# Kernel optimization log

Hardware: AMD Instinct MI355X
Metric: run time of the kernel (lower is better)

## Reference

```python
import jax, jax.numpy as jnp
import numpy as np

B, S, D = 4, 2048, 1024
H = 16
HD = D // H  # 64
BASE = 10000.0


def _rope_cache(seq_len, dim):
    inv_freq = 1.0 / (BASE ** (jnp.arange(0, dim, 2, dtype=jnp.float32) / dim))
    t = jnp.arange(seq_len, dtype=jnp.float32)
    freqs = jnp.einsum('i,j->ij', t, inv_freq)          # [S, dim/2]
    emb = jnp.concatenate([freqs, freqs], axis=-1)      # [S, dim]
    return jnp.cos(emb), jnp.sin(emb)


def _rotate_half(x):
    x1, x2 = jnp.split(x, 2, axis=-1)
    return jnp.concatenate([-x2, x1], axis=-1)


def setup_inputs() -> dict:
    key = jax.random.key(0)
    ks = jax.random.split(key, 5)
    scale = 1.0 / np.sqrt(D)
    return {
        'x': jax.random.normal(ks[0], (B, S, D), dtype=jnp.float32),
        'Wq': jax.random.normal(ks[1], (D, D), dtype=jnp.float32) * scale,
        'Wk': jax.random.normal(ks[2], (D, D), dtype=jnp.float32) * scale,
        'Wv': jax.random.normal(ks[3], (D, D), dtype=jnp.float32) * scale,
        'Wo': jax.random.normal(ks[4], (D, D), dtype=jnp.float32) * scale,
    }


def reference(x, Wq, Wk, Wv, Wo):
    b, s, d = x.shape
    # projections (torch Linear, no bias): y = x @ W.T
    q = (x @ Wq.T).reshape(b, s, H, HD).transpose(0, 2, 1, 3)  # [B,H,S,HD]
    k = (x @ Wk.T).reshape(b, s, H, HD).transpose(0, 2, 1, 3)
    v = (x @ Wv.T).reshape(b, s, H, HD).transpose(0, 2, 1, 3)
    cos, sin = _rope_cache(s, HD)  # [S, HD]
    cos = cos[None, None]
    sin = sin[None, None]
    q = q * cos + _rotate_half(q) * sin
    k = k * cos + _rotate_half(k) * sin
    scale = 1.0 / np.sqrt(HD)
    attn = jnp.einsum('bhqd,bhkd->bhqk', q, k) * scale  # [B,H,S,S]
    attn = jax.nn.softmax(attn, axis=-1)
    out = jnp.einsum('bhqk,bhkd->bhqd', attn, v)
    out = out.transpose(0, 2, 1, 3).reshape(b, s, d)
    return out @ Wo.T
```

## Files before the change

### kernel.cpp

```cpp
#include <hip/hip_runtime.h>
#include <math.h>
#include <stdint.h>

#define BB 4
#define SS 2048
#define DDIM 1024
#define HH 16
#define HD 64
#define QKVLD 3072
#define QSCALE (0.125f * 1.44269504089f)

typedef __bf16 bf16x8 __attribute__((ext_vector_type(8)));
typedef float f32x4 __attribute__((ext_vector_type(4)));
typedef float f32x16 __attribute__((ext_vector_type(16)));
typedef int i32x4 __attribute__((ext_vector_type(4)));

__device__ __forceinline__ unsigned short f2bf(float f) {
    union { float f; unsigned u; } v; v.f = f;
    unsigned r = (v.u + 0x7FFFu + ((v.u >> 16) & 1u)) >> 16;
    return (unsigned short)r;
}
__device__ __forceinline__ void gload_lds16(const unsigned short* g, unsigned char* s) {
    __builtin_amdgcn_global_load_lds(
        (const __attribute__((address_space(1))) unsigned int*)(g),
        (__attribute__((address_space(3))) unsigned int*)(s), 16, 0, 0);
}

__global__ void prep_all(const float* __restrict__ x,
                         const float* __restrict__ Wq, const float* __restrict__ Wk,
                         const float* __restrict__ Wv, const float* __restrict__ Wo,
                         unsigned short* __restrict__ xb,
                         unsigned short* __restrict__ wqkv, unsigned short* __restrict__ wob,
                         float* __restrict__ cosT, float* __restrict__ sinT) {
    int bid = blockIdx.x;
    if (bid < 8192) {
        int i = bid * 256 + threadIdx.x;
        float4 v = ((const float4*)x)[i];
        ushort4 o;
        o.x = f2bf(v.x); o.y = f2bf(v.y); o.z = f2bf(v.z); o.w = f2bf(v.w);
        ((ushort4*)xb)[i] = o;
    } else if (bid < 12288) {
        int i = (bid - 8192) * 256 + threadIdx.x;
        int mat = i >> 18;
        int off = i & 262143;
        const float* src = (mat == 0) ? Wq : (mat == 1) ? Wk : (mat == 2) ? Wv : Wo;
        unsigned short* dst = (mat < 3) ? (wqkv + (size_t)mat * 1048576) : wob;
        float4 v = ((const float4*)src)[off];
        ushort4 o;
        o.x = f2bf(v.x); o.y = f2bf(v.y); o.z = f2bf(v.z); o.w = f2bf(v.w);
        ((ushort4*)dst)[off] = o;
    } else {
        int idx = (bid - 12288) * 256 + threadIdx.x;
        int s = idx >> 5;
        int j = idx & 31;
        float invf = powf(10000.0f, -(float)j / 32.0f);
        float ang = (float)s * invf;
        cosT[idx] = cosf(ang);
        sinT[idx] = sinf(ang);
    }
}

__global__ __launch_bounds__(512) void gemm256_qkv(const unsigned short* __restrict__ A,
                                                   const unsigned short* __restrict__ Bm,
                                                   unsigned short* __restrict__ C,
                                                   const float* __restrict__ cosT,
                                                   const float* __restrict__ sinT,
                                                   unsigned short* __restrict__ vt) {
    __shared__ unsigned char smem[131072];
    const int t = threadIdx.x;
    const int l = t & 63;
    const int w = t >> 6;
    const int wm = w >> 2;
    const int wn = w & 3;
    const int K = DDIM;
    const int NT = K >> 6;

    const int bid = blockIdx.y * gridDim.x + blockIdx.x;
    const int cpx = (gridDim.x * gridDim.y) >> 3;
    const int swz = (bid & 7) * cpx + (bid >> 3);
    const int row0 = (swz / gridDim.x) * 256;
    const int col0 = (swz % gridDim.x) * 256;

    f32x4 acc[8][4];
#pragma unroll
    for (int i = 0; i < 8; ++i)
#pragma unroll
        for (int j = 0; j < 4; ++j) acc[i][j] = f32x4{0.f, 0.f, 0.f, 0.f};

    const unsigned short* aSg = A + (size_t)(row0 + w * 16 + (l >> 3)) * K + ((l & 7) ^ (l >> 3)) * 8;
    const unsigned short* bSg = Bm + (size_t)(col0 + w * 16 + (l >> 3)) * K + ((l & 7) ^ (l >> 3)) * 8;
    const int dRow = (w * 16) * 128;

#define STAGE_A(kt, h, j, buf) \
    gload_lds16(aSg + (size_t)((h) * 128 + (j) * 8) * K + (kt) * 64, \
                smem + (buf) * 65536 + (h) * 16384 + dRow + (j) * 1024)
#define STAGE_B(kt, h, j, buf) \
    gload_lds16(bSg + (size_t)((h) * 128 + (j) * 8) * K + (kt) * 64, \
                smem + (buf) * 65536 + 32768 + (h) * 16384 + dRow + (j) * 1024)

    STAGE_B(0, 0, 0, 0); STAGE_B(0, 0, 1, 0); STAGE_B(0, 1, 0, 0); STAGE_B(0, 1, 1, 0);
    STAGE_A(0, 0, 0, 0); STAGE_A(0, 0, 1, 0); STAGE_A(0, 1, 0, 0); STAGE_A(0, 1, 1, 0);
    STAGE_B(1, 0, 0, 1); STAGE_B(1, 0, 1, 1); STAGE_B(1, 1, 0, 1); STAGE_B(1, 1, 1, 1);
    asm volatile("s_waitcnt vmcnt(4)" ::: "memory");
    __builtin_amdgcn_s_barrier();

    const int cA = (l >> 4) << 4;
    const int swr = (l & 7) << 4;
    const int rA0 = wm * 128 + (l & 15);
    const int rB0 = wn * 64 + (l & 15);

    int cur = 0;
    for (int u = 0; u < NT; ++u) {
        const int nxt = cur ^ 1;
        const unsigned char* Ab = smem + cur * 65536;
        const unsigned char* Bb = smem + cur * 65536 + 32768;
        const bool pA = (u + 1 < NT);
        const bool pB = (u + 2 < NT);
        bf16x8 bfr[4][2];

#pragma unroll
        for (int p = 0; p < 4; ++p) {
            if (p == 0) { if (pA) { STAGE_A(u + 1, 0, 0, nxt); STAGE_A(u + 1, 0, 1, nxt); } }
            if (p == 1) { if (pA) { STAGE_A(u + 1, 1, 0, nxt); STAGE_A(u + 1, 1, 1, nxt); } }
            if (p == 2) { if (pB) { STAGE_B(u + 2, 0, 0, cur); STAGE_B(u + 2, 0, 1, cur); } }
            if (p == 3) { if (pB) { STAGE_B(u + 2, 1, 0, cur); STAGE_B(u + 2, 1, 1, cur); } }

            if (p == 0) {
#pragma unroll
                for (int ni = 0; ni < 4; ++ni)
#pragma unroll
                    for (int kk = 0; kk < 2; ++kk) {
                        int row = rB0 + ni * 16;
                        bfr[ni][kk] = *(const bf16x8*)(Bb + (row * 128 + ((kk * 64 + cA) ^ swr)));
                    }
            }
            bf16x8 af[2][2];
#pragma unroll
            for (int m2 = 0; m2 < 2; ++m2)
#pragma unroll
                for (int kk = 0; kk < 2; ++kk) {
                    int row = rA0 + (p * 2 + m2) * 16;
                    af[m2][kk] = *(const bf16x8*)(Ab + (row * 128 + ((kk * 64 + cA) ^ swr)));
                }

            __builtin_amdgcn_s_barrier();
            asm volatile("s_waitcnt lgkmcnt(0)" ::: "memory");
            __builtin_amdgcn_sched_barrier(0);
            __builtin_amdgcn_s_setprio(1);
#pragma unroll
            for (int m2 = 0; m2 < 2; ++m2)
#pragma unroll
                for (int ni = 0; ni < 4; ++ni)
#pragma unroll
                    for (int kk = 0; kk < 2; ++kk)
                        acc[p * 2 + m2][ni] = __builtin_amdgcn_mfma_f32_16x16x32_bf16(
                            af[m2][kk], bfr[ni][kk], acc[p * 2 + m2][ni], 0, 0, 0);
            __builtin_amdgcn_s_setprio(0);
            if (p == 3) {
                if (u < NT - 2) asm volatile("s_waitcnt vmcnt(4)" ::: "memory");
                else            asm volatile("s_waitcnt vmcnt(0)" ::: "memory");
            }
            __builtin_amdgcn_s_barrier();
        }
        cur = nxt;
    }
#undef STAGE_A
#undef STAGE_B

    const int cr = (l >> 4) << 2;
    const int cc = l & 15;
    const int sec = (col0 + wn * 64) >> 10;

    if (sec == 2) {
#pragma unroll
        for (int mi = 0; mi < 8; ++mi) {
            int s0 = row0 + wm * 128 + mi * 16 + cr;
            int bI = s0 >> 11;
            int sI = s0 & (SS - 1);
#pragma unroll
            for (int ni = 0; ni < 4; ++ni) {
                int vcol = col0 + wn * 64 + ni * 16 + cc - 2048;
                int hh = vcol >> 6, dd = vcol & 63;
                ushort4 o;
                o.x = f2bf(acc[mi][ni][0]);
                o.y = f2bf(acc[mi][ni][1]);
                o.z = f2bf(acc[mi][ni][2]);
                o.w = f2bf(acc[mi][ni][3]);
                *(ushort4*)&vt[((size_t)((bI * HH + hh) * HD + dd)) * SS + sI] = o;
            }
        }
    } else {
        const float qs = (sec == 0) ? QSCALE : 1.0f;
#pragma unroll
        for (int mi = 0; mi < 8; ++mi) {
#pragma unroll
            for (int r = 0; r < 4; ++r) {
                int grow = row0 + wm * 128 + mi * 16 + cr + r;
                int s = grow & (SS - 1);
#pragma unroll
                for (int ni = 0; ni < 2; ++ni) {
                    int j = ni * 16 + cc;
                    float c = cosT[(s << 5) + j];
                    float sn = sinT[(s << 5) + j];
                    float x1 = acc[mi][ni][r], x2 = acc[mi][ni + 2][r];
                    int gcol = col0 + wn * 64 + j;
                    C[(size_t)grow * QKVLD + gcol]      = f2bf((x1 * c - x2 * sn) * qs);
                    C[(size_t)grow * QKVLD + gcol + 32] = f2bf((x2 * c + x1 * sn) * qs);
                }
            }
        }
    }
}

__global__ __launch_bounds__(512) void gemm_out256(const unsigned short* __restrict__ A,
                                                   const unsigned short* __restrict__ Bm,
                                                   float* __restrict__ C) {
    __shared__ unsigned char smem[98304];
    const int t = threadIdx.x;
    const int l = t & 63;
    const int w = t >> 6;
    const int wm = w >> 2;
    const int wn = w & 3;
    const int K = DDIM;
    const int NT = K >> 6;

    const int bid = blockIdx.y * gridDim.x + blockIdx.x;
    const int cpx = (gridDim.x * gridDim.y) >> 3;
    const int swz = (bid & 7) * cpx + (bid >> 3);
    const int row0 = (swz / gridDim.x) * 256;
    const int col0 = (swz % gridDim.x) * 128;

    f32x4 acc[8][2];
#pragma unroll
    for (int i = 0; i < 8; ++i)
#pragma unroll
        for (int j = 0; j < 2; ++j) acc[i][j] = f32x4{0.f, 0.f, 0.f, 0.f};

    const unsigned short* aSg = A + (size_t)(row0 + w * 8 + (l >> 3)) * QKVLD + ((l & 7) ^ (l >> 3)) * 8;
    const unsigned short* bSg = Bm + (size_t)(col0 + w * 8 + (l >> 3)) * K + ((l & 7) ^ (l >> 3)) * 8;
    const int dRow = (w * 8) * 128;

#define SA(kt, c, buf) \
    gload_lds16(aSg + (size_t)((c) * 64) * QKVLD + (kt) * 64, \
                smem + (buf) * 49152 + (c) * 8192 + dRow)
#define SB(kt, c, buf) \
    gload_lds16(bSg + (size_t)((c) * 64) * K + (kt) * 64, \
                smem + (buf) * 49152 + 32768 + (c) * 8192 + dRow)

    SB(0, 0, 0); SB(0, 1, 0);
    SA(0, 0, 0); SA(0, 1, 0); SA(0, 2, 0); SA(0, 3, 0);
    SB(1, 0, 1); SB(1, 1, 1);
    asm volatile("s_waitcnt vmcnt(2)" ::: "memory");
    __builtin_amdgcn_s_barrier();

    const int cA = (l >> 4) << 4;
    const int swr = (l & 7) << 4;
    const int rA0 = wm * 128 + (l & 15);
    const int rB0 = wn * 32 + (l & 15);

    int cur = 0;
    for (int u = 0; u < NT; ++u) {
        const int nxt = cur ^ 1;
        const unsigned char* Ab = smem + cur * 49152;
        const unsigned char* Bb = smem + cur * 49152 + 32768;
        const bool pA = (u + 1 < NT);
        const bool pB = (u + 2 < NT);
        bf16x8 bfr[2][2];

#pragma unroll
        for (int p = 0; p < 4; ++p) {
            if (p == 0) { if (pA) { SA(u + 1, 0, nxt); SA(u + 1, 1, nxt); } }
            if (p == 1) { if (pA) { SA(u + 1, 2, nxt); SA(u + 1, 3, nxt); } }
            if (p == 2) { if (pB) { SB(u + 2, 0, cur); } }
            if (p == 3) { if (pB) { SB(u + 2, 1, cur); } }

            if (p == 0) {
#pragma unroll
                for (int ni = 0; ni < 2; ++ni)
#pragma unroll
                    for (int kk = 0; kk < 2; ++kk) {
                        int row = rB0 + ni * 16;
                        bfr[ni][kk] = *(const bf16x8*)(Bb + (row * 128 + ((kk * 64 + cA) ^ swr)));
                    }
            }
            bf16x8 af[2][2];
#pragma unroll
            for (int m2 = 0; m2 < 2; ++m2)
#pragma unroll
                for (int kk = 0; kk < 2; ++kk) {
                    int row = rA0 + (p * 2 + m2) * 16;
                    af[m2][kk] = *(const bf16x8*)(Ab + (row * 128 + ((kk * 64 + cA) ^ swr)));
                }

            __builtin_amdgcn_s_barrier();
            asm volatile("s_waitcnt lgkmcnt(0)" ::: "memory");
            __builtin_amdgcn_sched_barrier(0);
            __builtin_amdgcn_s_setprio(1);
#pragma unroll
            for (int m2 = 0; m2 < 2; ++m2)
#pragma unroll
                for (int ni = 0; ni < 2; ++ni)
#pragma unroll
                    for (int kk = 0; kk < 2; ++kk)
                        acc[p * 2 + m2][ni] = __builtin_amdgcn_mfma_f32_16x16x32_bf16(
                            af[m2][kk], bfr[ni][kk], acc[p * 2 + m2][ni], 0, 0, 0);
            __builtin_amdgcn_s_setprio(0);
            if (p == 3) {
                if (u < NT - 2) asm volatile("s_waitcnt vmcnt(2)" ::: "memory");
                else            asm volatile("s_waitcnt vmcnt(0)" ::: "memory");
            }
            __builtin_amdgcn_s_barrier();
        }
        cur = nxt;
    }
#undef SA
#undef SB

    const int cr = (l >> 4) << 2;
    const int cc = l & 15;
#pragma unroll
    for (int mi = 0; mi < 8; ++mi)
#pragma unroll
        for (int ni = 0; ni < 2; ++ni) {
            int gcol = col0 + wn * 32 + ni * 16 + cc;
#pragma unroll
            for (int r = 0; r < 4; ++r) {
                int grow = row0 + wm * 128 + mi * 16 + cr + r;
                C[(size_t)grow * DDIM + gcol] = acc[mi][ni][r];
            }
        }
}

__global__ __launch_bounds__(512) void attn_mfma12(const unsigned short* __restrict__ qkv,
                                                   const unsigned short* __restrict__ vt,
                                                   unsigned short* __restrict__ og) {
    __shared__ unsigned char smem[32768];
    const int tid = threadIdx.x;
    const int ln = tid & 63;
    const int w = tid >> 6;
    const int lq = ln & 31;
    const int hi = ln >> 5;

    const int did = blockIdx.x;
    const int b = did & 3;
    const int h = (did >> 2) & 15;
    const int qb0 = (did >> 6) << 8;

    const int headoff = h * HD;
    const size_t bS = (size_t)b * SS;

    bf16x8 qf[4];
    {
        const unsigned short* qsrc = qkv + (bS + qb0 + w * 32 + lq) * QKVLD + headoff + hi * 8;
#pragma unroll
        for (int dc = 0; dc < 4; ++dc)
            qf[dc] = *(const bf16x8*)(qsrc + dc * 16);
    }

    f32x16 oacc[2];
#pragma unroll
    for (int i = 0; i < 2; ++i)
#pragma unroll
        for (int r = 0; r < 16; ++r) oacc[i][r] = 0.f;
    float lsum = 0.f;

    f32x16 fzero;
#pragma unroll
    for (int r = 0; r < 16; ++r) fzero[r] = 0.f;

    const int srow = w * 8 + (ln >> 3);
    const int scol = ((ln & 7) ^ (ln >> 3)) << 3;
    const unsigned short* kbase_g = qkv + bS * QKVLD + 1024 + headoff;
    const unsigned short* vtbase_g = vt + (size_t)(b * HH + h) * HD * SS;

    {
        gload_lds16(kbase_g + (size_t)srow * QKVLD + scol, smem + w * 1024);
        gload_lds16(vtbase_g + (size_t)srow * SS + scol,   smem + 16384 + w * 1024);
    }
    __syncthreads();

#pragma unroll 2
    for (int tkv = 0; tkv < SS / 64; ++tkv) {
        const int cur = tkv & 1;
        const int kcur = cur * 8192;
        const int vcur = 16384 + cur * 8192;
        const int nxt = cur ^ 1;
        const bool pre = (tkv + 1 < SS / 64);
        if (pre) {
            const int kv1 = (tkv + 1) * 64;
            gload_lds16(kbase_g + (size_t)(kv1 + srow) * QKVLD + scol,
                        smem + nxt * 8192 + w * 1024);
            gload_lds16(vtbase_g + (size_t)srow * SS + kv1 + scol,
                        smem + 16384 + nxt * 8192 + w * 1024);
        }

        f32x16 st[2];
#pragma unroll
        for (int kb = 0; kb < 2; ++kb) {
            bf16x8 kf[4];
#pragma unroll
            for (int dc = 0; dc < 4; ++dc) {
                int row = kb * 32 + lq;
                int o = kcur + ((row * 128 + dc * 32 + hi * 16) ^ ((row & 7) << 4));
                kf[dc] = *(const bf16x8*)(smem + o);
            }
            __builtin_amdgcn_s_setprio(1);
            st[kb] = __builtin_amdgcn_mfma_f32_32x32x16_bf16(kf[0], qf[0], fzero, 0, 0, 0);
#pragma unroll
            for (int dc = 1; dc < 4; ++dc)
                st[kb] = __builtin_amdgcn_mfma_f32_32x32x16_bf16(kf[dc], qf[dc], st[kb], 0, 0, 0);
            __builtin_amdgcn_s_setprio(0);
        }

        float pg[32];
#pragma unroll
        for (int j = 0; j < 16; ++j) pg[j] = __builtin_amdgcn_exp2f(st[0][j]);
#pragma unroll
        for (int j = 0; j < 16; ++j) pg[16 + j] = __builtin_amdgcn_exp2f(st[1][j]);

        i32x4 pwv[4];
#pragma unroll
        for (int g = 0; g < 4; ++g) {
            unsigned u0, u1, u2, u3;
            asm("v_cvt_pk_bf16_f32 %0, %1, %2" : "=v"(u0) : "v"(pg[g * 8 + 0]), "v"(pg[g * 8 + 1]));
            asm("v_cvt_pk_bf16_f32 %0, %1, %2" : "=v"(u1) : "v"(pg[g * 8 + 2]), "v"(pg[g * 8 + 3]));
            asm("v_cvt_pk_bf16_f32 %0, %1, %2" : "=v"(u2) : "v"(pg[g * 8 + 4]), "v"(pg[g * 8 + 5]));
            asm("v_cvt_pk_bf16_f32 %0, %1, %2" : "=v"(u3) : "v"(pg[g * 8 + 6]), "v"(pg[g * 8 + 7]));
            asm("v_permlane32_swap_b32 %0, %1" : "+v"(u0), "+v"(u2));
            asm("v_permlane32_swap_b32 %0, %1" : "+v"(u1), "+v"(u3));
            pwv[g][0] = (int)u0; pwv[g][1] = (int)u1; pwv[g][2] = (int)u2; pwv[g][3] = (int)u3;
        }

        float rs;
        {
            float s0 = (pg[0] + pg[1]) + (pg[2] + pg[3]);
            float s1 = (pg[4] + pg[5]) + (pg[6] + pg[7]);
            float s2 = (pg[8] + pg[9]) + (pg[10] + pg[11]);
            float s3 = (pg[12] + pg[13]) + (pg[14] + pg[15]);
            float s4 = (pg[16] + pg[17]) + (pg[18] + pg[19]);
            float s5 = (pg[20] + pg[21]) + (pg[22] + pg[23]);
            float s6 = (pg[24] + pg[25]) + (pg[26] + pg[27]);
            float s7 = (pg[28] + pg[29]) + (pg[30] + pg[31]);
            rs = ((s0 + s1) + (s2 + s3)) + ((s4 + s5) + (s6 + s7));
        }
        rs += __shfl_xor(rs, 32);
        lsum += rs;

        __builtin_amdgcn_s_setprio(1);
#pragma unroll
        for (int dblk = 0; dblk < 2; ++dblk) {
#pragma unroll
            for (int ks = 0; ks < 4; ++ks) {
                int row = dblk * 32 + lq;
                int o = vcur + ((row * 128 + ks * 32 + hi * 16) ^ ((row & 7) << 4));
                bf16x8 vf = *(const bf16x8*)(smem + o);
                oacc[dblk] = __builtin_amdgcn_mfma_f32_32x32x16_bf16(
                    __builtin_bit_cast(bf16x8, pwv[ks]), vf, oacc[dblk], 0, 0, 0);
            }
        }
        __builtin_amdgcn_s_setprio(0);

        __syncthreads();
    }

    {
        float inv = 1.0f / lsum;
#pragma unroll
        for (int r = 0; r < 16; ++r) {
            int crow = (r & 3) + 8 * (r >> 2) + 4 * hi;
            float invr = __shfl(inv, crow);
            int grow = qb0 + w * 32 + crow;
            size_t base = (bS + grow) * QKVLD + headoff + lq;
            og[base]      = f2bf(oacc[0][r] * invr);
            og[base + 32] = f2bf(oacc[1][r] * invr);
        }
    }
}

extern "C" void kernel_launch(void* const* d_in, const int* in_sizes, int n_in,
                              void* d_out, int out_size, void* d_ws, size_t ws_size,
                              hipStream_t stream) {
    const float* x  = (const float*)d_in[0];
    const float* Wq = (const float*)d_in[1];
    const float* Wk = (const float*)d_in[2];
    const float* Wv = (const float*)d_in[3];
    const float* Wo = (const float*)d_in[4];
    float* out = (float*)d_out;

    const size_t BSD = (size_t)BB * SS * DDIM;
    const size_t WSZ = (size_t)DDIM * DDIM;

    unsigned short* xb   = (unsigned short*)d_ws;
    unsigned short* wqkv = xb + BSD;
    unsigned short* wob  = wqkv + 3 * WSZ;
    unsigned short* qkv  = wob + WSZ;
    unsigned short* vt   = qkv + (size_t)BB * SS * QKVLD;
    float* cosT = (float*)(vt + BSD);
    float* sinT = cosT + (size_t)SS * 32;

    hipLaunchKernelGGL(prep_all, dim3(12544), dim3(256), 0, stream,
                       x, Wq, Wk, Wv, Wo, xb, wqkv, wob, cosT, sinT);

    hipLaunchKernelGGL(gemm256_qkv, dim3(QKVLD / 256, BB * SS / 256), dim3(512), 0, stream,
                       xb, wqkv, qkv, cosT, sinT, vt);

    hipLaunchKernelGGL(attn_mfma12, dim3(512), dim3(512), 0, stream, qkv, vt, qkv);

    hipLaunchKernelGGL(gemm_out256, dim3(DDIM / 128, BB * SS / 256), dim3(512), 0, stream,
                       qkv, wob, out);
}
```

Baseline: 180.4 us.

## Shrink QKV GEMM tile to 256x128 with LDS exchange for RoPE pairs

Changes the QKV projection GEMM tile from 256x256 to 256x128, which doubles the grid to 768 blocks, halves the accumulator registers and cuts LDS from 128KB to 96KB. The aim is better occupancy and CU load balance on a 256-CU device, where 384 blocks would leave some CUs idle in the second wave. Because each wave now owns only 32 columns, the two RoPE halves of a head sit in neighbouring waves. The epilogue therefore swaps accumulators through LDS in two synchronized passes, which adds shared-memory traffic and barriers. The smaller tile also lowers arithmetic intensity per global load.

```diff
diff --git a/kernel.cpp b/kernel.cpp
--- a/kernel.cpp
+++ b/kernel.cpp
@@ -60,13 +60,13 @@
     }
 }
 
-__global__ __launch_bounds__(512) void gemm256_qkv(const unsigned short* __restrict__ A,
-                                                   const unsigned short* __restrict__ Bm,
-                                                   unsigned short* __restrict__ C,
-                                                   const float* __restrict__ cosT,
-                                                   const float* __restrict__ sinT,
-                                                   unsigned short* __restrict__ vt) {
-    __shared__ unsigned char smem[131072];
+__global__ __launch_bounds__(512) void gemm128b_qkv(const unsigned short* __restrict__ A,
+                                                    const unsigned short* __restrict__ Bm,
+                                                    unsigned short* __restrict__ C,
+                                                    const float* __restrict__ cosT,
+                                                    const float* __restrict__ sinT,
+                                                    unsigned short* __restrict__ vt) {
+    __shared__ unsigned char smem[98304];
     const int t = threadIdx.x;
     const int l = t & 63;
     const int w = t >> 6;
@@ -79,55 +79,55 @@
     const int cpx = (gridDim.x * gridDim.y) >> 3;
     const int swz = (bid & 7) * cpx + (bid >> 3);
     const int row0 = (swz / gridDim.x) * 256;
-    const int col0 = (swz % gridDim.x) * 256;
-
-    f32x4 acc[8][4];
+    const int col0 = (swz % gridDim.x) * 128;
+
+    f32x4 acc[8][2];
 #pragma unroll
     for (int i = 0; i < 8; ++i)
 #pragma unroll
-        for (int j = 0; j < 4; ++j) acc[i][j] = f32x4{0.f, 0.f, 0.f, 0.f};
-
-    const unsigned short* aSg = A + (size_t)(row0 + w * 16 + (l >> 3)) * K + ((l & 7) ^ (l >> 3)) * 8;
-    const unsigned short* bSg = Bm + (size_t)(col0 + w * 16 + (l >> 3)) * K + ((l & 7) ^ (l >> 3)) * 8;
-    const int dRow = (w * 16) * 128;
-
-#define STAGE_A(kt, h, j, buf) \
-    gload_lds16(aSg + (size_t)((h) * 128 + (j) * 8) * K + (kt) * 64, \
-                smem + (buf) * 65536 + (h) * 16384 + dRow + (j) * 1024)
-#define STAGE_B(kt, h, j, buf) \
-    gload_lds16(bSg + (size_t)((h) * 128 + (j) * 8) * K + (kt) * 64, \
-                smem + (buf) * 65536 + 32768 + (h) * 16384 + dRow + (j) * 1024)
-
-    STAGE_B(0, 0, 0, 0); STAGE_B(0, 0, 1, 0); STAGE_B(0, 1, 0, 0); STAGE_B(0, 1, 1, 0);
-    STAGE_A(0, 0, 0, 0); STAGE_A(0, 0, 1, 0); STAGE_A(0, 1, 0, 0); STAGE_A(0, 1, 1, 0);
-    STAGE_B(1, 0, 0, 1); STAGE_B(1, 0, 1, 1); STAGE_B(1, 1, 0, 1); STAGE_B(1, 1, 1, 1);
-    asm volatile("s_waitcnt vmcnt(4)" ::: "memory");
+        for (int j = 0; j < 2; ++j) acc[i][j] = f32x4{0.f, 0.f, 0.f, 0.f};
+
+    const unsigned short* aSg = A + (size_t)(row0 + w * 8 + (l >> 3)) * K + ((l & 7) ^ (l >> 3)) * 8;
+    const unsigned short* bSg = Bm + (size_t)(col0 + w * 8 + (l >> 3)) * K + ((l & 7) ^ (l >> 3)) * 8;
+    const int dRow = (w * 8) * 128;
+
+#define SA(kt, c, buf) \
+    gload_lds16(aSg + (size_t)((c) * 64) * K + (kt) * 64, \
+                smem + (buf) * 49152 + (c) * 8192 + dRow)
+#define SB(kt, c, buf) \
+    gload_lds16(bSg + (size_t)((c) * 64) * K + (kt) * 64, \
+                smem + (buf) * 49152 + 32768 + (c) * 8192 + dRow)
+
+    SB(0, 0, 0); SB(0, 1, 0);
+    SA(0, 0, 0); SA(0, 1, 0); SA(0, 2, 0); SA(0, 3, 0);
+    SB(1, 0, 1); SB(1, 1, 1);
+    asm volatile("s_waitcnt vmcnt(2)" ::: "memory");
     __builtin_amdgcn_s_barrier();
 
     const int cA = (l >> 4) << 4;
     const int swr = (l & 7) << 4;
     const int rA0 = wm * 128 + (l & 15);
-    const int rB0 = wn * 64 + (l & 15);
+    const int rB0 = wn * 32 + (l & 15);
 
     int cur = 0;
     for (int u = 0; u < NT; ++u) {
         const int nxt = cur ^ 1;
-        const unsigned char* Ab = smem + cur * 65536;
-        const unsigned char* Bb = smem + cur * 65536 + 32768;
+        const unsigned char* Ab = smem + cur * 49152;
+        const unsigned char* Bb = smem + cur * 49152 + 32768;
         const bool pA = (u + 1 < NT);
         const bool pB = (u + 2 < NT);
-        bf16x8 bfr[4][2];
+        bf16x8 bfr[2][2];
 
 #pragma unroll
         for (int p = 0; p < 4; ++p) {
-            if (p == 0) { if (pA) { STAGE_A(u + 1, 0, 0, nxt); STAGE_A(u + 1, 0, 1, nxt); } }
-            if (p == 1) { if (pA) { STAGE_A(u + 1, 1, 0, nxt); STAGE_A(u + 1, 1, 1, nxt); } }
-            if (p == 2) { if (pB) { STAGE_B(u + 2, 0, 0, cur); STAGE_B(u + 2, 0, 1, cur); } }
-            if (p == 3) { if (pB) { STAGE_B(u + 2, 1, 0, cur); STAGE_B(u + 2, 1, 1, cur); } }
+            if (p == 0) { if (pA) { SA(u + 1, 0, nxt); SA(u + 1, 1, nxt); } }
+            if (p == 1) { if (pA) { SA(u + 1, 2, nxt); SA(u + 1, 3, nxt); } }
+            if (p == 2) { if (pB) { SB(u + 2, 0, cur); } }
+            if (p == 3) { if (pB) { SB(u + 2, 1, cur); } }
 
             if (p == 0) {
 #pragma unroll
-                for (int ni = 0; ni < 4; ++ni)
+                for (int ni = 0; ni < 2; ++ni)
 #pragma unroll
                     for (int kk = 0; kk < 2; ++kk) {
                         int row = rB0 + ni * 16;
@@ -150,26 +150,26 @@
 #pragma unroll
             for (int m2 = 0; m2 < 2; ++m2)
 #pragma unroll
-                for (int ni = 0; ni < 4; ++ni)
+                for (int ni = 0; ni < 2; ++ni)
 #pragma unroll
                     for (int kk = 0; kk < 2; ++kk)
                         acc[p * 2 + m2][ni] = __builtin_amdgcn_mfma_f32_16x16x32_bf16(
                             af[m2][kk], bfr[ni][kk], acc[p * 2 + m2][ni], 0, 0, 0);
             __builtin_amdgcn_s_setprio(0);
             if (p == 3) {
-                if (u < NT - 2) asm volatile("s_waitcnt vmcnt(4)" ::: "memory");
+                if (u < NT - 2) asm volatile("s_waitcnt vmcnt(2)" ::: "memory");
                 else            asm volatile("s_waitcnt vmcnt(0)" ::: "memory");
             }
             __builtin_amdgcn_s_barrier();
         }
         cur = nxt;
     }
-#undef STAGE_A
-#undef STAGE_B
+#undef SA
+#undef SB
 
     const int cr = (l >> 4) << 2;
     const int cc = l & 15;
-    const int sec = (col0 + wn * 64) >> 10;
+    const int sec = col0 >> 10;
 
     if (sec == 2) {
 #pragma unroll
@@ -178,8 +178,8 @@
             int bI = s0 >> 11;
             int sI = s0 & (SS - 1);
 #pragma unroll
-            for (int ni = 0; ni < 4; ++ni) {
-                int vcol = col0 + wn * 64 + ni * 16 + cc - 2048;
+            for (int ni = 0; ni < 2; ++ni) {
+                int vcol = col0 + wn * 32 + ni * 16 + cc - 2048;
                 int hh = vcol >> 6, dd = vcol & 63;
                 ushort4 o;
                 o.x = f2bf(acc[mi][ni][0]);
@@ -191,21 +191,38 @@
         }
     } else {
         const float qs = (sec == 0) ? QSCALE : 1.0f;
-#pragma unroll
-        for (int mi = 0; mi < 8; ++mi) {
-#pragma unroll
-            for (int r = 0; r < 4; ++r) {
-                int grow = row0 + wm * 128 + mi * 16 + cr + r;
-                int s = grow & (SS - 1);
-#pragma unroll
-                for (int ni = 0; ni < 2; ++ni) {
-                    int j = ni * 16 + cc;
-                    float c = cosT[(s << 5) + j];
-                    float sn = sinT[(s << 5) + j];
-                    float x1 = acc[mi][ni][r], x2 = acc[mi][ni + 2][r];
-                    int gcol = col0 + wn * 64 + j;
-                    C[(size_t)grow * QKVLD + gcol]      = f2bf((x1 * c - x2 * sn) * qs);
-                    C[(size_t)grow * QKVLD + gcol + 32] = f2bf((x2 * c + x1 * sn) * qs);
+        const int pw = w ^ 1;
+        const bool hiHalf = (wn & 1);
+#pragma unroll
+        for (int pass = 0; pass < 2; ++pass) {
+            __syncthreads();
+#pragma unroll
+            for (int m4 = 0; m4 < 4; ++m4)
+#pragma unroll
+                for (int ni = 0; ni < 2; ++ni)
+#pragma unroll
+                    for (int r = 0; r < 4; ++r)
+                        *(float*)(smem + w * 8192 +
+                                  ((m4 * 16 + cr + r) * 128 + (ni * 16 + cc) * 4)) =
+                            acc[pass * 4 + m4][ni][r];
+            __syncthreads();
+#pragma unroll
+            for (int m4 = 0; m4 < 4; ++m4) {
+#pragma unroll
+                for (int r = 0; r < 4; ++r) {
+                    int rr = m4 * 16 + cr + r;
+                    int grow = row0 + wm * 128 + pass * 64 + rr;
+                    int s = grow & (SS - 1);
+#pragma unroll
+                    for (int ni = 0; ni < 2; ++ni) {
+                        int lc = ni * 16 + cc;
+                        float mine = acc[pass * 4 + m4][ni][r];
+                        float other = *(const float*)(smem + pw * 8192 + (rr * 128 + lc * 4));
+                        float c = cosT[(s << 5) + lc];
+                        float sn = sinT[(s << 5) + lc];
+                        float o = hiHalf ? (mine * c + other * sn) : (mine * c - other * sn);
+                        C[(size_t)grow * QKVLD + col0 + wn * 32 + lc] = f2bf(o * qs);
+                    }
                 }
             }
         }
@@ -501,7 +518,7 @@
     hipLaunchKernelGGL(prep_all, dim3(12544), dim3(256), 0, stream,
                        x, Wq, Wk, Wv, Wo, xb, wqkv, wob, cosT, sinT);
 
-    hipLaunchKernelGGL(gemm256_qkv, dim3(QKVLD / 256, BB * SS / 256), dim3(512), 0, stream,
+    hipLaunchKernelGGL(gemm128b_qkv, dim3(QKVLD / 128, BB * SS / 256), dim3(512), 0, stream,
                        xb, wqkv, qkv, cosT, sinT, vt);
 
     hipLaunchKernelGGL(attn_mfma12, dim3(512), dim3(512), 0, stream, qkv, vt, qkv);
```

New measurement: 184.0 us. +2.0%, slower.
